# Performance work log

Hardware: AMD Instinct MI355X
Metric: run time of the kernel (lower is better)

The kernel has to match this reference:

```python
import jax, jax.numpy as jnp
import numpy as np

V, E, H, CTX = 32000, 512, 1024, 1024
T, B = 64, 64

def setup_inputs() -> dict:
    key = jax.random.key(0)
    ks = jax.random.split(key, 16)
    s = lambda *sh: 1.0 / np.sqrt(sh[-1])
    inp = {
        "seq": jax.random.randint(ks[0], (T, B), 0, V, dtype=jnp.int32),
        "context": jax.random.normal(ks[1], (B, CTX), dtype=jnp.float32),
        "emb": jax.random.normal(ks[2], (V, E), dtype=jnp.float32) * 0.02,
        "W_ih": jax.random.normal(ks[3], (4 * H, E + CTX), dtype=jnp.float32) * s(E + CTX),
        "b_ih": jnp.zeros((4 * H,), dtype=jnp.float32),
        "W_hh": jax.random.normal(ks[4], (4 * H, H), dtype=jnp.float32) * s(H),
        "b_hh": jnp.zeros((4 * H,), dtype=jnp.float32),
        "W_initS": jax.random.normal(ks[5], (H, CTX), dtype=jnp.float32) * s(CTX),
        "b_initS": jnp.zeros((H,), dtype=jnp.float32),
        "W_initC": jax.random.normal(ks[6], (H, CTX), dtype=jnp.float32) * s(CTX),
        "b_initC": jnp.zeros((H,), dtype=jnp.float32),
        "W_d1": jax.random.normal(ks[7], (H, 2 * H), dtype=jnp.float32) * s(2 * H),
        "b_d1": jnp.zeros((H,), dtype=jnp.float32),
        "W_d2": jax.random.normal(ks[8], (V, H), dtype=jnp.float32) * s(H),
        "b_d2": jnp.zeros((V,), dtype=jnp.float32),
        "mode": 1,
    }
    return inp

def reference(seq, context, emb, W_ih, b_ih, W_hh, b_hh, W_initS, b_initS,
              W_initC, b_initC, W_d1, b_d1, W_d2, b_d2, mode):
    # init state from context (nonlinear = tanh); mode=1 -> eval path (no dropout)
    h0 = jnp.tanh(context @ W_initS.T + b_initS)  # [B,H]
    c0 = jnp.tanh(context @ W_initC.T + b_initC)  # [B,H]

    def step(carry, tok):
        h, c = carry
        x = jnp.concatenate([context, emb[tok]], axis=1)          # [B, CTX+E]
        gates = x @ W_ih.T + b_ih + h @ W_hh.T + b_hh             # [B, 4H]
        i_g, f_g, g_g, o_g = jnp.split(gates, 4, axis=1)
        c_new = jax.nn.sigmoid(f_g) * c + jax.nn.sigmoid(i_g) * jnp.tanh(g_g)
        h_new = jax.nn.sigmoid(o_g) * jnp.tanh(c_new)
        hid = jnp.tanh(jnp.concatenate([h_new, c_new], axis=1) @ W_d1.T + b_d1)  # [B,H]
        out = hid @ W_d2.T + b_d2                                  # [B,V]
        return (h_new, c_new), out

    _, outputs = jax.lax.scan(step, (h0, c0), seq)  # [T,B,V]
    return outputs
```

## Files before the change

kernel.cpp:

```cpp
#include <hip/hip_runtime.h>
#include <hip/hip_bf16.h>
#include <cstdint>

#define V_  32000
#define E_  512
#define H_  1024
#define CTX_ 1024
#define T_  64
#define B_  64
#define FH_ 4096
#define NRB 128

typedef __attribute__((ext_vector_type(8))) __bf16 bf16x8;
typedef __attribute__((ext_vector_type(4))) __bf16 bf16x4;
typedef __attribute__((ext_vector_type(4))) float f32x4;

#define DEV static __device__ __forceinline__

DEV __bf16 f2bf(float f) {
    union { float f; unsigned u; } v; v.f = f;
    unsigned r = (v.u + 0x7FFFu + ((v.u >> 16) & 1u)) >> 16;
    unsigned short s = (unsigned short)r;
    return __builtin_bit_cast(__bf16, s);
}

DEV float sigm(float x) { return 1.0f / (1.0f + __expf(-x)); }

DEV void st8cc(__bf16* p, unsigned long long v) {
    __hip_atomic_store((unsigned long long*)p, v,
                       __ATOMIC_RELAXED, __HIP_MEMORY_SCOPE_AGENT);
}

#define GL(g, l) __builtin_amdgcn_global_load_lds(                         \
    (const __attribute__((address_space(1))) void*)(g),                    \
    (__attribute__((address_space(3))) void*)(l), 16, 0, 0)

__global__ __launch_bounds__(256) void k_cast(const float* __restrict__ src,
                                              __bf16* __restrict__ dst, int n4) {
    int i = blockIdx.x * 256 + threadIdx.x;
    if (i >= n4) return;
    float4 v = *(const float4*)(src + (size_t)i * 4);
    bf16x4 o; o[0]=f2bf(v.x); o[1]=f2bf(v.y); o[2]=f2bf(v.z); o[3]=f2bf(v.w);
    *(bf16x4*)(dst + (size_t)i * 4) = o;
}

__global__ __launch_bounds__(256) void k_cast_wihe(const float* __restrict__ Wih,
                                                   __bf16* __restrict__ dst) {
    int i = blockIdx.x * 256 + threadIdx.x;
    int e = i * 4, j = e >> 9, k = e & 511;
    float4 v = *(const float4*)(Wih + (size_t)j * (CTX_ + E_) + CTX_ + k);
    bf16x4 o; o[0]=f2bf(v.x); o[1]=f2bf(v.y); o[2]=f2bf(v.z); o[3]=f2bf(v.w);
    *(bf16x4*)(dst + (size_t)e) = o;
}

__global__ __launch_bounds__(256) void k_gather_x(const int* __restrict__ seq,
                                                  const float* __restrict__ emb,
                                                  __bf16* __restrict__ dst) {
    int i = blockIdx.x * 256 + threadIdx.x;
    int e = i * 4, r = e >> 9, k = e & 511;
    int tok = seq[r];
    float4 v = *(const float4*)(emb + (size_t)tok * E_ + k);
    bf16x4 o; o[0]=f2bf(v.x); o[1]=f2bf(v.y); o[2]=f2bf(v.z); o[3]=f2bf(v.w);
    *(bf16x4*)(dst + (size_t)e) = o;
}

__global__ __launch_bounds__(256) void k_init(const float* __restrict__ ctx,
                                              const float* __restrict__ WS, const float* __restrict__ bS,
                                              const float* __restrict__ WC, const float* __restrict__ bC,
                                              __bf16* __restrict__ h0, float* __restrict__ c0) {
    int idx = blockIdx.x * 256 + threadIdx.x;
    int r = idx >> 4, bg = idx & 15;
    int sel = r >> 10, u = r & 1023;
    const float4* w = (const float4*)((sel ? WC : WS) + (size_t)u * CTX_);
    float acc[4] = {0.f,0.f,0.f,0.f};
    for (int k = 0; k < 256; ++k) {
        float4 wv = w[k];
#pragma unroll
        for (int i = 0; i < 4; ++i) {
            float4 cv = *(const float4*)(ctx + (size_t)(bg + 16*i) * CTX_ + k * 4);
            acc[i] += wv.x*cv.x + wv.y*cv.y + wv.z*cv.z + wv.w*cv.w;
        }
    }
    float bias = sel ? bC[u] : bS[u];
#pragma unroll
    for (int i = 0; i < 4; ++i) {
        int b = bg + 16*i;
        float v = tanhf(acc[i] + bias);
        if (sel) c0[(size_t)b * H_ + u] = v;
        else     h0[(size_t)b * 2048 + u] = f2bf(v);
    }
}

__global__ __launch_bounds__(256) void k_ctxgates(const float* __restrict__ ctx,
                                                  const float* __restrict__ Wih,
                                                  const float* __restrict__ bih,
                                                  const float* __restrict__ bhh,
                                                  float* __restrict__ out) {
    int idx = blockIdx.x * 256 + threadIdx.x;
    int j = idx >> 4, bg = idx & 15;
    const float4* w = (const float4*)(Wih + (size_t)j * (CTX_ + E_));
    float acc[4] = {0.f,0.f,0.f,0.f};
    for (int k = 0; k < 256; ++k) {
        float4 wv = w[k];
#pragma unroll
        for (int i = 0; i < 4; ++i) {
            float4 cv = *(const float4*)(ctx + (size_t)(bg + 16*i) * CTX_ + k * 4);
            acc[i] += wv.x*cv.x + wv.y*cv.y + wv.z*cv.z + wv.w*cv.w;
        }
    }
    float bias = bih[j] + bhh[j];
#pragma unroll
    for (int i = 0; i < 4; ++i) out[(size_t)(bg + 16*i) * FH_ + j] = acc[i] + bias;
}

__global__ __launch_bounds__(1024) void k_zero(unsigned* __restrict__ bar) {
    bar[threadIdx.x] = 0u;
}

__global__ __launch_bounds__(512, 2) void k_rnn(
    const __bf16* __restrict__ Whh, const __bf16* __restrict__ WihE,
    const __bf16* __restrict__ Xb, const float* __restrict__ ctxg,
    const float* __restrict__ c0,
    __bf16* __restrict__ HCx, unsigned* __restrict__ bar)
{
    __shared__ float red[8][64][36];
    __shared__ __bf16 hnb[64][8];
    __shared__ __bf16 cnb[64][8];
    const int tid = threadIdx.x;
    const int w = tid >> 6, lane = tid & 63;
    const int fr = lane & 15, fq = lane >> 4;
    const int u0 = (int)blockIdx.x * 8;
    const int kb = w * 192;

    bf16x8 breg[2][6];
#pragma unroll
    for (int ni = 0; ni < 2; ++ni) {
        const int n = ni * 16 + fr;
        const int j = (n >> 3) * H_ + u0 + (n & 7);
#pragma unroll
        for (int ks = 0; ks < 6; ++ks) {
            const int k = kb + ks * 32;
            const __bf16* src = (k < H_) ? (Whh + (size_t)j * H_ + k)
                                         : (WihE + (size_t)j * E_ + (k - H_));
            breg[ni][ks] = *(const bf16x8*)(src + fq * 8);
        }
    }
    const int cb = tid >> 3, cul = tid & 7, u = u0 + cul;
    float creg = c0[(size_t)cb * H_ + u];
    float cg[4];
#pragma unroll
    for (int g = 0; g < 4; ++g) cg[g] = ctxg[(size_t)cb * FH_ + g * H_ + u];

#pragma unroll 1
    for (int t = 0; t < T_; ++t) {
        const __bf16* hprev = HCx + (size_t)t * (B_ * 2 * H_);
        __bf16*       hcur  = HCx + (size_t)(t + 1) * (B_ * 2 * H_);
        const __bf16* Xt = Xb + (size_t)t * (B_ * E_);

        f32x4 acc[4][2];
#pragma unroll
        for (int mi = 0; mi < 4; ++mi)
#pragma unroll
            for (int ni = 0; ni < 2; ++ni) acc[mi][ni] = (f32x4){0.f,0.f,0.f,0.f};

#pragma unroll
        for (int ks = 0; ks < 6; ++ks) {
            const int k = kb + ks * 32;
            bf16x8 af[4];
#pragma unroll
            for (int mi = 0; mi < 4; ++mi) {
                const int row = mi * 16 + fr;
                const __bf16* src = (k < H_)
                    ? (hprev + (size_t)row * 2048 + k + fq * 8)
                    : (Xt + (size_t)row * E_ + (k - H_) + fq * 8);
                af[mi] = *(const bf16x8*)src;
            }
#pragma unroll
            for (int mi = 0; mi < 4; ++mi)
#pragma unroll
                for (int ni = 0; ni < 2; ++ni)
                    acc[mi][ni] = __builtin_amdgcn_mfma_f32_16x16x32_bf16(
                        af[mi], breg[ni][ks], acc[mi][ni], 0, 0, 0);
        }
#pragma unroll
        for (int mi = 0; mi < 4; ++mi)
#pragma unroll
            for (int ni = 0; ni < 2; ++ni)
#pragma unroll
                for (int r = 0; r < 4; ++r)
                    red[w][mi * 16 + fq * 4 + r][ni * 16 + fr] = acc[mi][ni][r];
        __syncthreads();

        float gv[4];
#pragma unroll
        for (int g = 0; g < 4; ++g) {
            float s = cg[g];
#pragma unroll
            for (int wv = 0; wv < 8; ++wv) s += red[wv][cb][g * 8 + cul];
            gv[g] = s;
        }
        const float cn = sigm(gv[1]) * creg + sigm(gv[0]) * tanhf(gv[2]);
        const float hn = sigm(gv[3]) * tanhf(cn);
        creg = cn;
        hnb[cb][cul] = f2bf(hn);
        cnb[cb][cul] = f2bf(cn);
        __syncthreads();

        if (tid < 256) {
            const int b = tid >> 2, sel = (tid >> 1) & 1, hf = tid & 1;
            const __bf16* s = sel ? &cnb[b][hf * 4] : &hnb[b][hf * 4];
            unsigned long long q = *(const unsigned long long*)s;
            st8cc(hcur + (size_t)b * 2048 + sel * H_ + u0 + hf * 4, q);
        }

        __syncthreads();
        if (tid == 0) {
            unsigned* b4 = bar + t * 16;
            __hip_atomic_fetch_add(b4, 1u, __ATOMIC_RELAXED, __HIP_MEMORY_SCOPE_AGENT);
            while (__hip_atomic_load(b4, __ATOMIC_RELAXED, __HIP_MEMORY_SCOPE_AGENT)
                   < (unsigned)NRB) { }
            __builtin_amdgcn_fence(__ATOMIC_ACQUIRE, "agent");
        }
        __syncthreads();
    }
}

DEV void xcd_tiles(int bid, int ntx, int nty, int& x, int& y) {
    const int xcd = bid & 7, i = bid >> 3;
    const int cy = nty >> 3;
    x = i / cy;
    y = xcd * cy + (i % cy);
}

__global__ __launch_bounds__(256) void k_gemm_d1(const __bf16* __restrict__ A,
                                                 const __bf16* __restrict__ Bt,
                                                 const float* __restrict__ bias,
                                                 __bf16* __restrict__ C,
                                                 int M, int N, int K) {
    __shared__ __align__(16) char smem[16384];
    __bf16* Als = (__bf16*)smem;
    __bf16* Bls = (__bf16*)(smem + 8192);
    const int tid = threadIdx.x, lane = tid & 63, wave = tid >> 6;
    const int wm = wave >> 1, wn = wave & 1;
    int tx, ty; xcd_tiles(blockIdx.x, N >> 7, M >> 7, tx, ty);
    const int bm = ty * 128, bn = tx * 128;
    const int srow = wave * 16 + (lane >> 2);
    const int scol = (lane & 3) * 8;
    const int fr = lane & 15, fq = lane >> 4;

    f32x4 acc[4][4];
#pragma unroll
    for (int i = 0; i < 4; ++i)
#pragma unroll
        for (int j = 0; j < 4; ++j) acc[i][j] = (f32x4){0.f,0.f,0.f,0.f};

    const int nkt = K >> 5;
    for (int kt = 0; kt < nkt; ++kt) {
        const int k0 = kt << 5;
        GL(A  + (size_t)(bm + srow) * K + k0 + scol,      smem + wave * 1024);
        GL(A  + (size_t)(bm + 64 + srow) * K + k0 + scol, smem + 4096 + wave * 1024);
        GL(Bt + (size_t)(bn + srow) * K + k0 + scol,      smem + 8192 + wave * 1024);
        GL(Bt + (size_t)(bn + 64 + srow) * K + k0 + scol, smem + 12288 + wave * 1024);
        __syncthreads();
        bf16x8 af[4], bfr[4];
#pragma unroll
        for (int mi = 0; mi < 4; ++mi)
            af[mi] = *(const bf16x8*)(Als + (wm*64 + mi*16 + fr) * 32 + fq * 8);
#pragma unroll
        for (int ni = 0; ni < 4; ++ni)
            bfr[ni] = *(const bf16x8*)(Bls + (wn*64 + ni*16 + fr) * 32 + fq * 8);
#pragma unroll
        for (int mi = 0; mi < 4; ++mi)
#pragma unroll
            for (int ni = 0; ni < 4; ++ni)
                acc[mi][ni] = __builtin_amdgcn_mfma_f32_16x16x32_bf16(af[mi], bfr[ni], acc[mi][ni], 0, 0, 0);
        __syncthreads();
    }
    const int cr = fq * 4, cc = fr;
#pragma unroll
    for (int ni = 0; ni < 4; ++ni) {
        const int gc = bn + wn*64 + ni*16 + cc;
        const float bv = bias[gc];
#pragma unroll
        for (int mi = 0; mi < 4; ++mi) {
            const int gr = bm + wm*64 + mi*16 + cr;
#pragma unroll
            for (int r = 0; r < 4; ++r)
                C[(size_t)(gr + r) * N + gc] = f2bf(tanhf(acc[mi][ni][r] + bv));
        }
    }
}

__global__ __launch_bounds__(256) void k_gemm_bt(const __bf16* __restrict__ A,
                                                 const __bf16* __restrict__ Bt,
                                                 const float* __restrict__ bias,
                                                 float* __restrict__ C,
                                                 int M, int N, int K) {
    __shared__ __align__(16) char smem[16384];
    __bf16* Als = (__bf16*)smem;
    __bf16* Bls = (__bf16*)(smem + 8192);
    const int tid = threadIdx.x, lane = tid & 63, wave = tid >> 6;
    const int wm = wave >> 1, wn = wave & 1;
    int tx, ty; xcd_tiles(blockIdx.x, N >> 7, M >> 7, tx, ty);
    const int bm = ty * 128, bn = tx * 128;
    const int srow = wave * 16 + (lane >> 2);
    const int scol = (lane & 3) * 8;
    const int fr = lane & 15, fq = lane >> 4;

    f32x4 acc[4][4];
#pragma unroll
    for (int i = 0; i < 4; ++i)
#pragma unroll
        for (int j = 0; j < 4; ++j) acc[i][j] = (f32x4){0.f,0.f,0.f,0.f};

    const int nkt = K >> 5;
    for (int kt = 0; kt < nkt; ++kt) {
        const int k0 = kt << 5;
        GL(A  + (size_t)(bm + srow) * K + k0 + scol,      smem + wave * 1024);
        GL(A  + (size_t)(bm + 64 + srow) * K + k0 + scol, smem + 4096 + wave * 1024);
        GL(Bt + (size_t)(bn + srow) * K + k0 + scol,      smem + 8192 + wave * 1024);
        GL(Bt + (size_t)(bn + 64 + srow) * K + k0 + scol, smem + 12288 + wave * 1024);
        __syncthreads();
        bf16x8 af[4], bfr[4];
#pragma unroll
        for (int mi = 0; mi < 4; ++mi)
            af[mi] = *(const bf16x8*)(Als + (wm*64 + mi*16 + fr) * 32 + fq * 8);
#pragma unroll
        for (int ni = 0; ni < 4; ++ni)
            bfr[ni] = *(const bf16x8*)(Bls + (wn*64 + ni*16 + fr) * 32 + fq * 8);
#pragma unroll
        for (int mi = 0; mi < 4; ++mi)
#pragma unroll
            for (int ni = 0; ni < 4; ++ni)
                acc[mi][ni] = __builtin_amdgcn_mfma_f32_16x16x32_bf16(af[mi], bfr[ni], acc[mi][ni], 0, 0, 0);
        __syncthreads();
    }
    const int cr = fq * 4, cc = fr;
#pragma unroll
    for (int ni = 0; ni < 4; ++ni) {
        const int gc = bn + wn*64 + ni*16 + cc;
        const float bv = bias ? bias[gc] : 0.f;
#pragma unroll
        for (int mi = 0; mi < 4; ++mi) {
            const int gr = bm + wm*64 + mi*16 + cr;
            float* cp = C + (size_t)gr * N + gc;
#pragma unroll
            for (int r = 0; r < 4; ++r) cp[(size_t)r * N] = acc[mi][ni][r] + bv;
        }
    }
}

extern "C" void kernel_launch(void* const* d_in, const int* in_sizes, int n_in,
                              void* d_out, int out_size, void* d_ws, size_t ws_size,
                              hipStream_t stream) {
    const int*   seq     = (const int*)d_in[0];
    const float* ctx     = (const float*)d_in[1];
    const float* emb     = (const float*)d_in[2];
    const float* W_ih    = (const float*)d_in[3];
    const float* b_ih    = (const float*)d_in[4];
    const float* W_hh    = (const float*)d_in[5];
    const float* b_hh    = (const float*)d_in[6];
    const float* W_initS = (const float*)d_in[7];
    const float* b_initS = (const float*)d_in[8];
    const float* W_initC = (const float*)d_in[9];
    const float* b_initC = (const float*)d_in[10];
    const float* W_d1    = (const float*)d_in[11];
    const float* b_d1    = (const float*)d_in[12];
    const float* W_d2    = (const float*)d_in[13];
    const float* b_d2    = (const float*)d_in[14];
    float* out = (float*)d_out;

    char* ws = (char*)d_ws;
    __bf16* Whh_bf  = (__bf16*)(ws + 0);
    __bf16* WihE_bf = (__bf16*)(ws + (8u << 20));
    __bf16* Wd1_bf  = (__bf16*)(ws + (12u << 20));
    __bf16* Wd2_bf  = (__bf16*)(ws + (16u << 20));
    __bf16* X_bf    = (__bf16*)(ws + 82313216u);
    float*  ctxg    = (float*) (ws + 86507520u);
    float*  cbuf    = (float*) (ws + 87556096u);
    __bf16* HCx     = (__bf16*)(ws + 87818240u);
    unsigned* bar   = (unsigned*)(ws + 104857600u);
    __bf16* hid     = (__bf16*)(ws + 0);

    k_cast<<<4096, 256, 0, stream>>>(W_hh, Whh_bf, 1048576);
    k_cast_wihe<<<2048, 256, 0, stream>>>(W_ih, WihE_bf);
    k_cast<<<2048, 256, 0, stream>>>(W_d1, Wd1_bf, 524288);
    k_cast<<<32000, 256, 0, stream>>>(W_d2, Wd2_bf, 8192000);
    k_gather_x<<<2048, 256, 0, stream>>>(seq, emb, X_bf);
    k_init<<<128, 256, 0, stream>>>(ctx, W_initS, b_initS, W_initC, b_initC, HCx, cbuf);
    k_ctxgates<<<256, 256, 0, stream>>>(ctx, W_ih, b_ih, b_hh, ctxg);
    k_zero<<<1, 1024, 0, stream>>>(bar);

    k_rnn<<<NRB, 512, 0, stream>>>(Whh_bf, WihE_bf, X_bf, ctxg, cbuf, HCx, bar);

    k_gemm_d1<<<(H_ / 128) * ((T_ * B_) / 128), 256, 0, stream>>>(
        HCx + (size_t)B_ * 2 * H_, Wd1_bf, b_d1, hid, T_ * B_, H_, 2 * H_);

    k_gemm_bt<<<(V_ / 128) * ((T_ * B_) / 128), 256, 0, stream>>>(
        hid, Wd2_bf, b_d2, out, T_ * B_, V_, H_);
}
```

Baseline: 2.013 ms.

## Split RNN grid barrier into arrive/wait and overlap next-step input GEMM

The per-step grid barrier becomes a two-level counter: blocks increment a per-group counter of 8 blocks, and the last arriver bumps a global counter. Each block now waits at the start of the next step instead of right after arriving. In the gap, each block computes the embedding-input MFMA contribution for step t+1, moving the X·W_ih work off the serial critical path and shortening the contended atomic spin. The acquire fence after the wait is removed, so visibility of the previous h/c across XCD caches now rests on the coherent stores and the relaxed loads alone.

```diff
diff --git a/kernel.cpp b/kernel.cpp
--- a/kernel.cpp
+++ b/kernel.cpp
@@ -113,8 +113,9 @@
     for (int i = 0; i < 4; ++i) out[(size_t)(bg + 16*i) * FH_ + j] = acc[i] + bias;
 }
 
-__global__ __launch_bounds__(1024) void k_zero(unsigned* __restrict__ bar) {
-    bar[threadIdx.x] = 0u;
+__global__ __launch_bounds__(256) void k_zero(unsigned* __restrict__ bar, int n) {
+    int i = blockIdx.x * 256 + threadIdx.x;
+    if (i < n) bar[i] = 0u;
 }
 
 __global__ __launch_bounds__(512, 2) void k_rnn(
@@ -130,20 +131,20 @@
     const int w = tid >> 6, lane = tid & 63;
     const int fr = lane & 15, fq = lane >> 4;
     const int u0 = (int)blockIdx.x * 8;
-    const int kb = w * 192;
-
-    bf16x8 breg[2][6];
+    const int kh  = w * 128;
+    const int kxo = w * 64;
+
+    bf16x8 bregh[2][4], bregx[2][2];
 #pragma unroll
     for (int ni = 0; ni < 2; ++ni) {
         const int n = ni * 16 + fr;
         const int j = (n >> 3) * H_ + u0 + (n & 7);
 #pragma unroll
-        for (int ks = 0; ks < 6; ++ks) {
-            const int k = kb + ks * 32;
-            const __bf16* src = (k < H_) ? (Whh + (size_t)j * H_ + k)
-                                         : (WihE + (size_t)j * E_ + (k - H_));
-            breg[ni][ks] = *(const bf16x8*)(src + fq * 8);
-        }
+        for (int ks = 0; ks < 4; ++ks)
+            bregh[ni][ks] = *(const bf16x8*)(Whh + (size_t)j * H_ + kh + ks * 32 + fq * 8);
+#pragma unroll
+        for (int ks = 0; ks < 2; ++ks)
+            bregx[ni][ks] = *(const bf16x8*)(WihE + (size_t)j * E_ + kxo + ks * 32 + fq * 8);
     }
     const int cb = tid >> 3, cul = tid & 7, u = u0 + cul;
     float creg = c0[(size_t)cb * H_ + u];
@@ -151,36 +152,53 @@
 #pragma unroll
     for (int g = 0; g < 4; ++g) cg[g] = ctxg[(size_t)cb * FH_ + g * H_ + u];
 
+    f32x4 acc[4][2];
+#pragma unroll
+    for (int mi = 0; mi < 4; ++mi)
+#pragma unroll
+        for (int ni = 0; ni < 2; ++ni) acc[mi][ni] = (f32x4){0.f,0.f,0.f,0.f};
+
+#pragma unroll
+    for (int ks = 0; ks < 2; ++ks) {
+        bf16x8 af[4];
+#pragma unroll
+        for (int mi = 0; mi < 4; ++mi)
+            af[mi] = *(const bf16x8*)(Xb + (size_t)(mi * 16 + fr) * E_ + kxo + ks * 32 + fq * 8);
+#pragma unroll
+        for (int mi = 0; mi < 4; ++mi)
+#pragma unroll
+            for (int ni = 0; ni < 2; ++ni)
+                acc[mi][ni] = __builtin_amdgcn_mfma_f32_16x16x32_bf16(
+                    af[mi], bregx[ni][ks], acc[mi][ni], 0, 0, 0);
+    }
+
+    const int grp = (int)blockIdx.x >> 3;
+
 #pragma unroll 1
     for (int t = 0; t < T_; ++t) {
+        if (t > 0) {
+            if (tid == 0) {
+                unsigned* rp = bar + (size_t)(t - 1) * 272 + 256;
+                while (__hip_atomic_load(rp, __ATOMIC_RELAXED, __HIP_MEMORY_SCOPE_AGENT)
+                       < (unsigned)(NRB / 8)) { }
+            }
+            __syncthreads();
+        }
         const __bf16* hprev = HCx + (size_t)t * (B_ * 2 * H_);
         __bf16*       hcur  = HCx + (size_t)(t + 1) * (B_ * 2 * H_);
-        const __bf16* Xt = Xb + (size_t)t * (B_ * E_);
-
-        f32x4 acc[4][2];
-#pragma unroll
-        for (int mi = 0; mi < 4; ++mi)
-#pragma unroll
-            for (int ni = 0; ni < 2; ++ni) acc[mi][ni] = (f32x4){0.f,0.f,0.f,0.f};
-
-#pragma unroll
-        for (int ks = 0; ks < 6; ++ks) {
-            const int k = kb + ks * 32;
+
+#pragma unroll
+        for (int ks = 0; ks < 4; ++ks) {
             bf16x8 af[4];
 #pragma unroll
-            for (int mi = 0; mi < 4; ++mi) {
-                const int row = mi * 16 + fr;
-                const __bf16* src = (k < H_)
-                    ? (hprev + (size_t)row * 2048 + k + fq * 8)
-                    : (Xt + (size_t)row * E_ + (k - H_) + fq * 8);
-                af[mi] = *(const bf16x8*)src;
-            }
+            for (int mi = 0; mi < 4; ++mi)
+                af[mi] = *(const bf16x8*)(hprev + (size_t)(mi * 16 + fr) * 2048 + kh + ks * 32 + fq * 8);
 #pragma unroll
             for (int mi = 0; mi < 4; ++mi)
 #pragma unroll
                 for (int ni = 0; ni < 2; ++ni)
                     acc[mi][ni] = __builtin_amdgcn_mfma_f32_16x16x32_bf16(
-                        af[mi], breg[ni][ks], acc[mi][ni], 0, 0, 0);
+                        af[mi], bregh[ni][ks], acc[mi][ni], 0, 0, 0);
         }
 #pragma unroll
         for (int mi = 0; mi < 4; ++mi)
@@ -212,16 +230,37 @@
             unsigned long long q = *(const unsigned long long*)s;
             st8cc(hcur + (size_t)b * 2048 + sel * H_ + u0 + hf * 4, q);
         }
-
-        __syncthreads();
+        __syncthreads();
+
         if (tid == 0) {
-            unsigned* b4 = bar + t * 16;
-            __hip_atomic_fetch_add(b4, 1u, __ATOMIC_RELAXED, __HIP_MEMORY_SCOPE_AGENT);
-            while (__hip_atomic_load(b4, __ATOMIC_RELAXED, __HIP_MEMORY_SCOPE_AGENT)
-                   < (unsigned)NRB) { }
-            __builtin_amdgcn_fence(__ATOMIC_ACQUIRE, "agent");
-        }
-        __syncthreads();
+            unsigned* bs = bar + (size_t)t * 272;
+            unsigned old = __hip_atomic_fetch_add(bs + grp * 16, 1u,
+                               __ATOMIC_RELAXED, __HIP_MEMORY_SCOPE_AGENT);
+            if (old == 7u)
+                __hip_atomic_fetch_add(bs + 256, 1u,
+                    __ATOMIC_RELAXED, __HIP_MEMORY_SCOPE_AGENT);
+        }
+
+#pragma unroll
+        for (int mi = 0; mi < 4; ++mi)
+#pragma unroll
+            for (int ni = 0; ni < 2; ++ni) acc[mi][ni] = (f32x4){0.f,0.f,0.f,0.f};
+        if (t < T_ - 1) {
+            const __bf16* Xt = Xb + (size_t)(t + 1) * (B_ * E_);
+#pragma unroll
+            for (int ks = 0; ks < 2; ++ks) {
+                bf16x8 af[4];
+#pragma unroll
+                for (int mi = 0; mi < 4; ++mi)
+                    af[mi] = *(const bf16x8*)(Xt + (size_t)(mi * 16 + fr) * E_ + kxo + ks * 32 + fq * 8);
+#pragma unroll
+                for (int mi = 0; mi < 4; ++mi)
+#pragma unroll
+                    for (int ni = 0; ni < 2; ++ni)
+                        acc[mi][ni] = __builtin_amdgcn_mfma_f32_16x16x32_bf16(
+                            af[mi], bregx[ni][ks], acc[mi][ni], 0, 0, 0);
+            }
+        }
     }
 }
 
@@ -389,7 +428,7 @@
     k_gather_x<<<2048, 256, 0, stream>>>(seq, emb, X_bf);
     k_init<<<128, 256, 0, stream>>>(ctx, W_initS, b_initS, W_initC, b_initC, HCx, cbuf);
     k_ctxgates<<<256, 256, 0, stream>>>(ctx, W_ih, b_ih, b_hh, ctxg);
-    k_zero<<<1, 1024, 0, stream>>>(bar);
+    k_zero<<<68, 256, 0, stream>>>(bar, 64 * 272);
 
     k_rnn<<<NRB, 512, 0, stream>>>(Whh_bf, WihE_bf, X_bf, ctxg, cbuf, HCx, bar);
 
```

Measured after the change: 1.854 ms. 1.09x faster.
